# Performance work log

Measured on AMD Instinct MI355X. Metric: run time of the kernel, lower is better.

The kernel has to match this reference:

```python
import jax, jax.numpy as jnp
import numpy as np

B = 2048
F = 267          # frame_size
L = 32           # latent_size
H = 256          # hidden_size (hard-coded in module)
E = 8            # num_experts
G = 64           # gate hidden size (hard-coded)
IN0 = L + F      # decoder layer0 input (latent + frame*cond_frames)
IN1 = L + H      # decoder inter input
OUT = F          # num_future_predictions * frame_size


def _lin_init(key, out_dim, in_dim):
    # kaiming-uniform-like scale
    bound = float(np.sqrt(1.0 / in_dim))
    return jax.random.uniform(key, (out_dim, in_dim), jnp.float32, -bound, bound)


def setup_inputs() -> dict:
    key = jax.random.key(0)
    ks = jax.random.split(key, 24)
    d = {}
    d["x"] = jax.random.normal(ks[0], (B, F), jnp.float32)
    d["c"] = jax.random.normal(ks[1], (B, F), jnp.float32)
    # encoder
    d["fc1_w"] = _lin_init(ks[2], H, 2 * F); d["fc1_b"] = jnp.zeros((H,), jnp.float32)
    d["fc2_w"] = _lin_init(ks[3], H, F + H); d["fc2_b"] = jnp.zeros((H,), jnp.float32)
    d["mu_w"] = _lin_init(ks[4], L, F + H);  d["mu_b"] = jnp.zeros((L,), jnp.float32)
    d["lv_w"] = _lin_init(ks[5], L, F + H);  d["lv_b"] = jnp.zeros((L,), jnp.float32)
    # gate
    d["g0_w"] = _lin_init(ks[6], G, IN0); d["g0_b"] = jnp.zeros((G,), jnp.float32)
    d["g1_w"] = _lin_init(ks[7], G, G);   d["g1_b"] = jnp.zeros((G,), jnp.float32)
    d["g2_w"] = _lin_init(ks[8], E, G);   d["g2_b"] = jnp.zeros((E,), jnp.float32)
    # expert weights [E, in, out], biases [E, out], bias filled 0.01 as in module
    d["w0"] = jax.random.uniform(ks[9], (E, IN0, H), jnp.float32, -1, 1) * np.sqrt(1.0 / IN0)
    d["b0"] = jnp.full((E, H), 0.01, jnp.float32)
    d["w1"] = jax.random.uniform(ks[10], (E, IN1, H), jnp.float32, -1, 1) * np.sqrt(1.0 / IN1)
    d["b1"] = jnp.full((E, H), 0.01, jnp.float32)
    d["w2"] = jax.random.uniform(ks[11], (E, IN1, OUT), jnp.float32, -1, 1) * np.sqrt(1.0 / IN1)
    d["b2"] = jnp.full((E, OUT), 0.01, jnp.float32)
    return d


def reference(x, c, fc1_w, fc1_b, fc2_w, fc2_b, mu_w, mu_b, lv_w, lv_b,
              g0_w, g0_b, g1_w, g1_b, g2_w, g2_b, w0, b0, w1, b1, w2, b2):
    elu = jax.nn.elu
    # ---- encoder ----
    h1 = elu(jnp.concatenate([x, c], axis=1) @ fc1_w.T + fc1_b)
    h2 = elu(jnp.concatenate([x, h1], axis=1) @ fc2_w.T + fc2_b)
    s = jnp.concatenate([x, h2], axis=1)
    mu = s @ mu_w.T + mu_b
    logvar = s @ lv_w.T + lv_b
    eps = jax.random.normal(jax.random.key(42), mu.shape, mu.dtype)
    z = mu + eps * jnp.exp(0.5 * logvar)
    # ---- mixed decoder ----
    g = elu(jnp.concatenate([z, c], axis=1) @ g0_w.T + g0_b)
    g = elu(g @ g1_w.T + g1_b)
    coeff = jax.nn.softmax(g @ g2_w.T + g2_b, axis=1)  # [B, E]
    layer_out = c
    for (W, bvec, act) in ((w0, b0, True), (w1, b1, True), (w2, b2, False)):
        inp = jnp.concatenate([z, layer_out], axis=1)          # [B, in]
        # per-expert GEMM then coefficient mixing (same math as per-sample
        # mixed-weight bmm: coeff @ flat_weight then baddbmm)
        out = jnp.einsum('be,bi,eio->bo', coeff, inp, W, optimize=True)
        out = out + coeff @ bvec                               # mixed bias
        layer_out = elu(out) if act else out
    return (layer_out, mu, logvar)
```

## Files before the change

kernel.cpp:

```cpp
#include <hip/hip_runtime.h>
#include <math.h>
#include <stdint.h>

#define DI __device__ __forceinline__

typedef __attribute__((ext_vector_type(8))) short bf16x8;
typedef __attribute__((ext_vector_type(4))) float f32x4;
typedef __attribute__((ext_vector_type(4))) int i32x4;

DI float elu_f(float v) { return v > 0.f ? v : expm1f(v); }

DI unsigned short f2bf(float f) {
  uint32_t u = __float_as_uint(f);
  return (unsigned short)((u + 0x7FFFu + ((u >> 16) & 1u)) >> 16);
}

DI void threefry2x32(uint32_t k0, uint32_t k1, uint32_t& x0, uint32_t& x1) {
  uint32_t ks0 = k0, ks1 = k1, ks2 = k0 ^ k1 ^ 0x1BD11BDAu;
  x0 += ks0; x1 += ks1;
#define TFR(r) { x0 += x1; x1 = (x1 << r) | (x1 >> (32 - r)); x1 ^= x0; }
  TFR(13) TFR(15) TFR(26) TFR(6)   x0 += ks1; x1 += ks2 + 1u;
  TFR(17) TFR(29) TFR(16) TFR(24)  x0 += ks2; x1 += ks0 + 2u;
  TFR(13) TFR(15) TFR(26) TFR(6)   x0 += ks0; x1 += ks1 + 3u;
  TFR(17) TFR(29) TFR(16) TFR(24)  x0 += ks1; x1 += ks2 + 4u;
  TFR(13) TFR(15) TFR(26) TFR(6)   x0 += ks2; x1 += ks0 + 5u;
#undef TFR
}

DI float erfinv_f(float x) {
  float w = -logf((1.0f - x) * (1.0f + x));
  float p;
  if (w < 5.0f) {
    w -= 2.5f;
    p = 2.81022636e-08f;
    p = fmaf(p, w, 3.43273939e-07f);
    p = fmaf(p, w, -3.5233877e-06f);
    p = fmaf(p, w, -4.39150654e-06f);
    p = fmaf(p, w, 0.00021858087f);
    p = fmaf(p, w, -0.00125372503f);
    p = fmaf(p, w, -0.00417768164f);
    p = fmaf(p, w, 0.246640727f);
    p = fmaf(p, w, 1.50140941f);
  } else {
    w = sqrtf(w) - 3.0f;
    p = -0.000200214257f;
    p = fmaf(p, w, 0.000100950558f);
    p = fmaf(p, w, 0.00134934322f);
    p = fmaf(p, w, -0.00367342844f);
    p = fmaf(p, w, 0.00573950773f);
    p = fmaf(p, w, -0.0076224613f);
    p = fmaf(p, w, 0.00943887047f);
    p = fmaf(p, w, 1.00167406f);
    p = fmaf(p, w, 2.83297682f);
  }
  return p * x;
}

struct MegaArgs {
  const float *x, *c;
  const float *fc1w, *fc1b, *fc2w, *fc2b, *muw, *mub, *lvw, *lvb;
  const float *g0w, *g0b, *g1w, *g1b, *g2w, *g2b;
  const float *w0, *b0, *w1, *b1, *w2, *b2;
  unsigned short *Ax, *Axh, *Axh2, *A0, *A1, *A2;
  unsigned short *fc1t, *fc2t, *mlvt, *g0t, *g1t, *w0b, *w1b, *w2b;
  float *cf, *outY, *outMu, *outLv;
};

template <int KT, int NE, int D, bool ELU, bool OUTF32>
__global__ __launch_bounds__(128, 2)
void pipe32(const unsigned short* __restrict__ A,
            const unsigned short* __restrict__ Wt, int N,
            const float* __restrict__ bias,
            const float* __restrict__ cfp,
            unsigned short* __restrict__ Cb, int ldcb, int cb_off,
            float* __restrict__ Cf) {
  constexpr int Kp = KT * 32, TT = NE * KT;
  __shared__ float bias_s[NE * 32];
  __shared__ float cfs[(NE > 1) ? 256 : 1];
  const int tid = threadIdx.x, lane = tid & 63, wv = tid >> 6;
  const int q = lane >> 4, l16 = lane & 15;
  const int m0 = blockIdx.x * 32;
  const int n0 = blockIdx.y * 32 + wv * 16;
  const int gc = n0 + l16;
  const int wrow = (gc < N) ? gc : (N - 1);
  const unsigned short* wlane = Wt + (size_t)wrow * Kp + q * 8;

  bf16x8 ring[D];
#pragma unroll
  for (int g = 0; g < D; g++) {
    if (g < TT) {
      int e = g / KT, c = g % KT;
      ring[g] = *(const bf16x8*)(wlane + (size_t)e * N * Kp + c * 32);
    }
  }
  bf16x8 areg[2][KT];
#pragma unroll
  for (int t = 0; t < 2; t++) {
    const unsigned short* alane = A + (size_t)(m0 + t * 16 + l16) * Kp + q * 8;
#pragma unroll
    for (int c = 0; c < KT; c++) areg[t][c] = *(const bf16x8*)(alane + c * 32);
  }

  if (NE == 1) {
    if (tid < 32) {
      int col = blockIdx.y * 32 + tid;
      bias_s[tid] = (col < N) ? bias[col] : 0.f;
    }
  } else {
    for (int idx = tid; idx < NE * 32; idx += 128) {
      int e = idx >> 5, col = blockIdx.y * 32 + (idx & 31);
      bias_s[idx] = (col < N) ? bias[(size_t)e * N + col] : 0.f;
    }
    for (int idx = tid; idx < 256; idx += 128)
      cfs[idx] = cfp[(size_t)(m0 + (idx >> 3)) * 8 + (idx & 7)];
  }
  __syncthreads();

  f32x4 acc[2] = {{0.f, 0.f, 0.f, 0.f}, {0.f, 0.f, 0.f, 0.f}};
  f32x4 accF[2] = {{0.f, 0.f, 0.f, 0.f}, {0.f, 0.f, 0.f, 0.f}};
#pragma unroll
  for (int g = 0; g < TT; g++) {
    const int e = g / KT, c = g % KT;
    bf16x8 bv = ring[g % D];
    acc[0] = __builtin_amdgcn_mfma_f32_16x16x32_bf16(areg[0][c], bv, acc[0], 0, 0, 0);
    acc[1] = __builtin_amdgcn_mfma_f32_16x16x32_bf16(areg[1][c], bv, acc[1], 0, 0, 0);
    if (g + D < TT) {
      int e2 = (g + D) / KT, c2 = (g + D) % KT;
      ring[g % D] = *(const bf16x8*)(wlane + (size_t)e2 * N * Kp + c2 * 32);
    }
    if (NE > 1 && c == KT - 1) {
      float bv2 = bias_s[e * 32 + wv * 16 + l16];
#pragma unroll
      for (int t = 0; t < 2; t++)
#pragma unroll
        for (int r = 0; r < 4; r++) {
          float ce = cfs[(t * 16 + q * 4 + r) * 8 + e];
          accF[t][r] += ce * (acc[t][r] + bv2);
          acc[t][r] = 0.f;
        }
    }
  }

  if (gc < N) {
#pragma unroll
    for (int t = 0; t < 2; t++)
#pragma unroll
      for (int r = 0; r < 4; r++) {
        int row = m0 + t * 16 + q * 4 + r;
        float v = (NE > 1) ? accF[t][r] : (acc[t][r] + bias_s[wv * 16 + l16]);
        if (ELU) v = elu_f(v);
        if (OUTF32) Cf[(size_t)row * 267 + gc] = v;
        else Cb[(size_t)row * ldcb + cb_off + gc] = f2bf(v);
      }
  }
}

__global__ __launch_bounds__(256) void k_prep(MegaArgs a) {
  __shared__ __align__(16) unsigned short T[64][72];
  const int bb = blockIdx.x, tid = threadIdx.x;
  if (bb < 512) {
    for (int rr = 0; rr < 4; rr++) {
      int b = bb * 4 + rr;
      const float* xr = a.x + (size_t)b * 267;
      const float* cr = a.c + (size_t)b * 267;
      unsigned short* axr = a.Ax + (size_t)b * 544;
      for (int k = tid; k < 544; k += 256) {
        float v = (k < 267) ? xr[k] : ((k < 534) ? cr[k - 267] : 0.f);
        axr[k] = f2bf(v);
      }
      unsigned short* ahr = a.Axh + (size_t)b * 544;
      unsigned short* ah2 = a.Axh2 + (size_t)b * 544;
      for (int k = tid; k < 267; k += 256) { unsigned short v = f2bf(xr[k]); ahr[k] = v; ah2[k] = v; }
      for (int k = 523 + tid; k < 544; k += 256) { ahr[k] = 0; ah2[k] = 0; }
      unsigned short* a0r = a.A0 + (size_t)b * 320;
      for (int k = tid; k < 288; k += 256)
        a0r[32 + k] = (k < 267) ? f2bf(cr[k]) : (unsigned short)0;
    }
  } else if (bb < 1152) {
    int r = bb - 512;
    const float* src; unsigned short* dst; int Ks, Kp2;
    if (r < 256)      { src = a.fc1w + (size_t)r * 534; dst = a.fc1t + (size_t)r * 544; Ks = 534; Kp2 = 544; }
    else if (r < 512) { int n = r - 256; src = a.fc2w + (size_t)n * 523; dst = a.fc2t + (size_t)n * 544; Ks = 523; Kp2 = 544; }
    else if (r < 576) { int n = r - 512; src = (n < 32) ? (a.muw + (size_t)n * 523) : (a.lvw + (size_t)(n - 32) * 523);
                        dst = a.mlvt + (size_t)n * 544; Ks = 523; Kp2 = 544; }
    else              { int n = r - 576; src = a.g0w + (size_t)n * 299; dst = a.g0t + (size_t)n * 320; Ks = 299; Kp2 = 320; }
    for (int k = tid; k < Kp2; k += 256) dst[k] = (k < Ks) ? f2bf(src[k]) : (unsigned short)0;
  } else if (bb == 1152) {
    for (int k = tid; k < 4096; k += 256) a.g1t[k] = f2bf(a.g1w[k]);
  } else {
    int t = bb - 1153;
    const float* W; unsigned short* D; int K, N2, Kp2, ldW, e, kt, nt;
    if (t < 160)      { e = t / 20;  int lt = t % 20;  kt = lt / 4; nt = lt % 4; W = a.w0; D = a.w0b; K = 299; N2 = 256; Kp2 = 320; ldW = 256; }
    else if (t < 320) { int u = t - 160; e = u / 20; int lt = u % 20; kt = lt / 4; nt = lt % 4; W = a.w1; D = a.w1b; K = 288; N2 = 256; Kp2 = 288; ldW = 256; }
    else              { int u = t - 320; e = u / 25; int lt = u % 25; kt = lt / 5; nt = lt % 5; W = a.w2; D = a.w2b; K = 288; N2 = 267; Kp2 = 288; ldW = 267; }
    const int k0 = kt * 64, n0 = nt * 64;
    const float* We = W + (size_t)e * K * ldW;
    const int jj = tid & 63, ii0 = tid >> 6;
#pragma unroll
    for (int p = 0; p < 16; p++) {
      int i = ii0 + p * 4;
      int gk = k0 + i, gn = n0 + jj;
      float v = (gk < K && gn < N2) ? We[(size_t)gk * ldW + gn] : 0.f;
      T[jj][i] = f2bf(v);
    }
    __syncthreads();
    int j = tid >> 2, chb = tid & 3;
    int gn = n0 + j;
    if (gn < N2) {
      unsigned short* drow = D + ((size_t)e * N2 + gn) * Kp2 + k0;
#pragma unroll
      for (int s = 0; s < 2; s++) {
        int ch = chb + s * 4;
        if (k0 + ch * 8 < Kp2) {
          i32x4 v = *(i32x4*)(&T[j][ch * 8]);
          *(i32x4*)(drow + ch * 8) = v;
        }
      }
    }
  }
}

__global__ __launch_bounds__(256, 2) void k_mulv_gate(MegaArgs a) {
  __shared__ float mlvS[16 * 65];
  __shared__ __align__(16) unsigned short A0p[16 * 328];
  __shared__ __align__(16) unsigned short gaB[16 * 72];
  __shared__ __align__(16) unsigned short g1B[64 * 72];
  __shared__ float g2wT[64 * 8];
  __shared__ float gB[16 * 65];
  __shared__ float lg[16 * 8];
  const int tid = threadIdx.x, lane = tid & 63, wid = tid >> 6;
  const int q = lane >> 4, l16 = lane & 15;
  const int m0 = blockIdx.x * 16;
  const int cl = wid * 16 + l16;

  const unsigned short* alane = a.Axh2 + (size_t)(m0 + l16) * 544 + q * 8;
  const unsigned short* wlA = a.mlvt + (size_t)cl * 544 + q * 8;
  bf16x8 ring[8];
#pragma unroll
  for (int g = 0; g < 8; g++) ring[g] = *(const bf16x8*)(wlA + g * 32);
  bf16x8 areg[17];
#pragma unroll
  for (int c = 0; c < 17; c++) areg[c] = *(const bf16x8*)(alane + c * 32);
  f32x4 acc = {0.f, 0.f, 0.f, 0.f};
#pragma unroll
  for (int g = 0; g < 17; g++) {
    acc = __builtin_amdgcn_mfma_f32_16x16x32_bf16(areg[g], ring[g % 8], acc, 0, 0, 0);
    if (g + 8 < 17) ring[g % 8] = *(const bf16x8*)(wlA + (g + 8) * 32);
  }
#pragma unroll
  for (int r = 0; r < 4; r++) mlvS[(q * 4 + r) * 65 + cl] = acc[r];
  for (int idx = tid; idx < 576; idx += 256) {
    int row = idx / 36, ch = 4 + idx % 36;
    *(i32x4*)(A0p + row * 328 + ch * 8) =
        *(const i32x4*)(a.A0 + (size_t)(m0 + row) * 320 + ch * 8);
  }
  if (tid < 16) { i32x4 z4 = {0, 0, 0, 0}; *(i32x4*)(A0p + tid * 328 + 320) = z4; }
  for (int idx = tid; idx < 512; idx += 256) {
    int row = idx >> 3, ch = idx & 7;
    *(i32x4*)(g1B + row * 72 + ch * 8) = *(const i32x4*)(a.g1t + (size_t)row * 64 + ch * 8);
  }
  for (int idx = tid; idx < 512; idx += 256)
    g2wT[(idx & 63) * 8 + (idx >> 6)] = a.g2w[idx];
  __syncthreads();

  {
    const int m = tid >> 4, j0 = (tid & 15) * 2, R = m0 + m;
#pragma unroll
    for (int jj = 0; jj < 2; jj++) {
      int j = j0 + jj;
      float mu = mlvS[m * 65 + j] + a.mub[j];
      float lvv = mlvS[m * 65 + j + 32] + a.lvb[j];
      uint32_t x0 = 0u, x1 = (uint32_t)(R * 32 + j);
      threefry2x32(0u, 42u, x0, x1);
      uint32_t bits = x0 ^ x1;
      float f = __uint_as_float((bits >> 9) | 0x3F800000u) - 1.0f;
      const float lo = -0.99999994039535522461f;
      float u = fmaf(f, 2.0f, lo);
      u = fmaxf(u, lo);
      float eps = 1.41421356237f * erfinv_f(u);
      float z = fmaf(eps, expf(0.5f * lvv), mu);
      a.outMu[(size_t)R * 32 + j] = mu;
      a.outLv[(size_t)R * 32 + j] = lvv;
      unsigned short zb = f2bf(z);
      A0p[m * 328 + j] = zb;
      a.A0[(size_t)R * 320 + j] = zb;
      a.A1[(size_t)R * 288 + j] = zb;
      a.A2[(size_t)R * 288 + j] = zb;
    }
  }
  __syncthreads();

  const unsigned short* wlC = a.g0t + (size_t)cl * 320 + q * 8;
  bf16x8 ring2[8];
#pragma unroll
  for (int g = 0; g < 8; g++) ring2[g] = *(const bf16x8*)(wlC + g * 32);
  f32x4 accC = {0.f, 0.f, 0.f, 0.f};
#pragma unroll
  for (int g = 0; g < 10; g++) {
    bf16x8 av = *(const bf16x8*)(A0p + l16 * 328 + g * 32 + q * 8);
    accC = __builtin_amdgcn_mfma_f32_16x16x32_bf16(av, ring2[g % 8], accC, 0, 0, 0);
    if (g + 8 < 10) ring2[g % 8] = *(const bf16x8*)(wlC + (g + 8) * 32);
  }
  {
    float bc = a.g0b[cl];
#pragma unroll
    for (int r = 0; r < 4; r++)
      gaB[(q * 4 + r) * 72 + cl] = f2bf(elu_f(accC[r] + bc));
  }
  __syncthreads();

  f32x4 accD = {0.f, 0.f, 0.f, 0.f};
#pragma unroll
  for (int tau = 0; tau < 2; tau++) {
    bf16x8 av = *(const bf16x8*)(gaB + l16 * 72 + tau * 32 + q * 8);
    bf16x8 bv = *(const bf16x8*)(g1B + cl * 72 + tau * 32 + q * 8);
    accD = __builtin_amdgcn_mfma_f32_16x16x32_bf16(av, bv, accD, 0, 0, 0);
  }
  {
    float bc = a.g1b[cl];
#pragma unroll
    for (int r = 0; r < 4; r++)
      gB[(q * 4 + r) * 65 + cl] = elu_f(accD[r] + bc);
  }
  __syncthreads();

  if (tid < 128) {
    int r = tid >> 3, e = tid & 7;
    float d = a.g2b[e];
#pragma unroll 8
    for (int k = 0; k < 64; k++) d = fmaf(gB[r * 65 + k], g2wT[k * 8 + e], d);
    lg[r * 8 + e] = d;
  }
  __syncthreads();
  if (tid < 16) {
    float mx = lg[tid * 8];
#pragma unroll
    for (int e2 = 1; e2 < 8; e2++) mx = fmaxf(mx, lg[tid * 8 + e2]);
    float s = 0.f, ex[8];
#pragma unroll
    for (int e2 = 0; e2 < 8; e2++) { ex[e2] = expf(lg[tid * 8 + e2] - mx); s += ex[e2]; }
    float inv = 1.f / s;
#pragma unroll
    for (int e2 = 0; e2 < 8; e2++) a.cf[(size_t)(m0 + tid) * 8 + e2] = ex[e2] * inv;
  }
}

extern "C" void kernel_launch(void* const* d_in, const int* in_sizes, int n_in,
                              void* d_out, int out_size, void* d_ws, size_t ws_size,
                              hipStream_t stream) {
  (void)in_sizes; (void)n_in; (void)out_size; (void)ws_size;
  float* out = (float*)d_out;
  float* ws = (float*)d_ws;

  MegaArgs a;
  a.x    = (const float*)d_in[0];
  a.c    = (const float*)d_in[1];
  a.fc1w = (const float*)d_in[2];  a.fc1b = (const float*)d_in[3];
  a.fc2w = (const float*)d_in[4];  a.fc2b = (const float*)d_in[5];
  a.muw  = (const float*)d_in[6];  a.mub  = (const float*)d_in[7];
  a.lvw  = (const float*)d_in[8];  a.lvb  = (const float*)d_in[9];
  a.g0w  = (const float*)d_in[10]; a.g0b  = (const float*)d_in[11];
  a.g1w  = (const float*)d_in[12]; a.g1b  = (const float*)d_in[13];
  a.g2w  = (const float*)d_in[14]; a.g2b  = (const float*)d_in[15];
  a.w0   = (const float*)d_in[16]; a.b0   = (const float*)d_in[17];
  a.w1   = (const float*)d_in[18]; a.b1   = (const float*)d_in[19];
  a.w2   = (const float*)d_in[20]; a.b2   = (const float*)d_in[21];

  a.outY  = out;
  a.outMu = out + 2048 * 267;
  a.outLv = a.outMu + 2048 * 32;

  a.Ax   = (unsigned short*)(ws);
  a.Axh  = (unsigned short*)(ws + 557056);
  a.Axh2 = (unsigned short*)(ws + 1114112);
  a.A0   = (unsigned short*)(ws + 1671168);
  a.A1   = (unsigned short*)(ws + 1998848);
  a.A2   = (unsigned short*)(ws + 2293760);
  a.fc1t = (unsigned short*)(ws + 2588672);
  a.fc2t = (unsigned short*)(ws + 2658304);
  a.mlvt = (unsigned short*)(ws + 2727936);
  a.g0t  = (unsigned short*)(ws + 2745344);
  a.g1t  = (unsigned short*)(ws + 2755584);
  a.w0b  = (unsigned short*)(ws + 2757632);
  a.w1b  = (unsigned short*)(ws + 3085312);
  a.w2b  = (unsigned short*)(ws + 3380224);
  a.cf   = ws + 3687808;

  dim3 blkP(256), blkG(128);
  k_prep<<<1673, blkP, 0, stream>>>(a);
  pipe32<17, 1, 12, true, false><<<dim3(64, 8), blkG, 0, stream>>>(
      a.Ax, a.fc1t, 256, a.fc1b, nullptr, a.Axh, 544, 267, nullptr);
  pipe32<17, 1, 12, true, false><<<dim3(64, 8), blkG, 0, stream>>>(
      a.Axh, a.fc2t, 256, a.fc2b, nullptr, a.Axh2, 544, 267, nullptr);
  k_mulv_gate<<<128, blkP, 0, stream>>>(a);
  pipe32<10, 8, 12, true, false><<<dim3(64, 8), blkG, 0, stream>>>(
      a.A0, a.w0b, 256, a.b0, a.cf, a.A1, 288, 32, nullptr);
  pipe32<9, 8, 12, true, false><<<dim3(64, 8), blkG, 0, stream>>>(
      a.A1, a.w1b, 256, a.b1, a.cf, a.A2, 288, 32, nullptr);
  pipe32<9, 8, 12, false, true><<<dim3(64, 9), blkG, 0, stream>>>(
      a.A2, a.w2b, 267, a.b2, a.cf, nullptr, 0, 0, a.outY);
}
```

Before: 175.8 us.

## Fuse encoder, gate, and expert decoder layers into one per-row-block kernel

Replaces the separate encoder GEMMs, mu/logvar+gate kernel, and three expert-mix GEMM launches with a single kernel that keeps each 16-row block's activations in shared memory across all layers. This removes intermediate global round-trips, launch gaps, and the redundant activation staging in the prep kernel. In exchange the grid shrinks to 128 blocks, reducing parallelism, and every block rereads all expert weights from cache.

```diff
diff --git a/kernel.cpp b/kernel.cpp
--- a/kernel.cpp
+++ b/kernel.cpp
@@ -7,6 +7,8 @@
 typedef __attribute__((ext_vector_type(8))) short bf16x8;
 typedef __attribute__((ext_vector_type(4))) float f32x4;
 typedef __attribute__((ext_vector_type(4))) int i32x4;
+
+#define MFMA16(av, bv, acc) __builtin_amdgcn_mfma_f32_16x16x32_bf16(av, bv, acc, 0, 0, 0)
 
 DI float elu_f(float v) { return v > 0.f ? v : expm1f(v); }
 
@@ -66,95 +68,6 @@
   float *cf, *outY, *outMu, *outLv;
 };
 
-template <int KT, int NE, int D, bool ELU, bool OUTF32>
-__global__ __launch_bounds__(128, 2)
-void pipe32(const unsigned short* __restrict__ A,
-            const unsigned short* __restrict__ Wt, int N,
-            const float* __restrict__ bias,
-            const float* __restrict__ cfp,
-            unsigned short* __restrict__ Cb, int ldcb, int cb_off,
-            float* __restrict__ Cf) {
-  constexpr int Kp = KT * 32, TT = NE * KT;
-  __shared__ float bias_s[NE * 32];
-  __shared__ float cfs[(NE > 1) ? 256 : 1];
-  const int tid = threadIdx.x, lane = tid & 63, wv = tid >> 6;
-  const int q = lane >> 4, l16 = lane & 15;
-  const int m0 = blockIdx.x * 32;
-  const int n0 = blockIdx.y * 32 + wv * 16;
-  const int gc = n0 + l16;
-  const int wrow = (gc < N) ? gc : (N - 1);
-  const unsigned short* wlane = Wt + (size_t)wrow * Kp + q * 8;
-
-  bf16x8 ring[D];
-#pragma unroll
-  for (int g = 0; g < D; g++) {
-    if (g < TT) {
-      int e = g / KT, c = g % KT;
-      ring[g] = *(const bf16x8*)(wlane + (size_t)e * N * Kp + c * 32);
-    }
-  }
-  bf16x8 areg[2][KT];
-#pragma unroll
-  for (int t = 0; t < 2; t++) {
-    const unsigned short* alane = A + (size_t)(m0 + t * 16 + l16) * Kp + q * 8;
-#pragma unroll
-    for (int c = 0; c < KT; c++) areg[t][c] = *(const bf16x8*)(alane + c * 32);
-  }
-
-  if (NE == 1) {
-    if (tid < 32) {
-      int col = blockIdx.y * 32 + tid;
-      bias_s[tid] = (col < N) ? bias[col] : 0.f;
-    }
-  } else {
-    for (int idx = tid; idx < NE * 32; idx += 128) {
-      int e = idx >> 5, col = blockIdx.y * 32 + (idx & 31);
-      bias_s[idx] = (col < N) ? bias[(size_t)e * N + col] : 0.f;
-    }
-    for (int idx = tid; idx < 256; idx += 128)
-      cfs[idx] = cfp[(size_t)(m0 + (idx >> 3)) * 8 + (idx & 7)];
-  }
-  __syncthreads();
-
-  f32x4 acc[2] = {{0.f, 0.f, 0.f, 0.f}, {0.f, 0.f, 0.f, 0.f}};
-  f32x4 accF[2] = {{0.f, 0.f, 0.f, 0.f}, {0.f, 0.f, 0.f, 0.f}};
-#pragma unroll
-  for (int g = 0; g < TT; g++) {
-    const int e = g / KT, c = g % KT;
-    bf16x8 bv = ring[g % D];
-    acc[0] = __builtin_amdgcn_mfma_f32_16x16x32_bf16(areg[0][c], bv, acc[0], 0, 0, 0);
-    acc[1] = __builtin_amdgcn_mfma_f32_16x16x32_bf16(areg[1][c], bv, acc[1], 0, 0, 0);
-    if (g + D < TT) {
-      int e2 = (g + D) / KT, c2 = (g + D) % KT;
-      ring[g % D] = *(const bf16x8*)(wlane + (size_t)e2 * N * Kp + c2 * 32);
-    }
-    if (NE > 1 && c == KT - 1) {
-      float bv2 = bias_s[e * 32 + wv * 16 + l16];
-#pragma unroll
-      for (int t = 0; t < 2; t++)
-#pragma unroll
-        for (int r = 0; r < 4; r++) {
-          float ce = cfs[(t * 16 + q * 4 + r) * 8 + e];
-          accF[t][r] += ce * (acc[t][r] + bv2);
-          acc[t][r] = 0.f;
-        }
-    }
-  }
-
-  if (gc < N) {
-#pragma unroll
-    for (int t = 0; t < 2; t++)
-#pragma unroll
-      for (int r = 0; r < 4; r++) {
-        int row = m0 + t * 16 + q * 4 + r;
-        float v = (NE > 1) ? accF[t][r] : (acc[t][r] + bias_s[wv * 16 + l16]);
-        if (ELU) v = elu_f(v);
-        if (OUTF32) Cf[(size_t)row * 267 + gc] = v;
-        else Cb[(size_t)row * ldcb + cb_off + gc] = f2bf(v);
-      }
-  }
-}
-
 __global__ __launch_bounds__(256) void k_prep(MegaArgs a) {
   __shared__ __align__(16) unsigned short T[64][72];
   const int bb = blockIdx.x, tid = threadIdx.x;
@@ -168,10 +81,6 @@
         float v = (k < 267) ? xr[k] : ((k < 534) ? cr[k - 267] : 0.f);
         axr[k] = f2bf(v);
       }
-      unsigned short* ahr = a.Axh + (size_t)b * 544;
-      unsigned short* ah2 = a.Axh2 + (size_t)b * 544;
-      for (int k = tid; k < 267; k += 256) { unsigned short v = f2bf(xr[k]); ahr[k] = v; ah2[k] = v; }
-      for (int k = 523 + tid; k < 544; k += 256) { ahr[k] = 0; ah2[k] = 0; }
       unsigned short* a0r = a.A0 + (size_t)b * 320;
       for (int k = tid; k < 288; k += 256)
         a0r[32 + k] = (k < 267) ? f2bf(cr[k]) : (unsigned short)0;
@@ -220,56 +129,117 @@
   }
 }
 
-__global__ __launch_bounds__(256, 2) void k_mulv_gate(MegaArgs a) {
-  __shared__ float mlvS[16 * 65];
-  __shared__ __align__(16) unsigned short A0p[16 * 328];
-  __shared__ __align__(16) unsigned short gaB[16 * 72];
-  __shared__ __align__(16) unsigned short g1B[64 * 72];
-  __shared__ float g2wT[64 * 8];
-  __shared__ float gB[16 * 65];
-  __shared__ float lg[16 * 8];
-  const int tid = threadIdx.x, lane = tid & 63, wid = tid >> 6;
+__global__ __launch_bounds__(512, 2) void k_chain(MegaArgs a) {
+  __shared__ __align__(16) unsigned short sAxh[16][552];
+  __shared__ __align__(16) unsigned short sA0[16][328];
+  __shared__ __align__(16) unsigned short sA1[16][296];
+  __shared__ float sMlv[16][65];
+  __shared__ __align__(16) unsigned short sGa[16][72];
+  __shared__ float sGb[16][65];
+  __shared__ float sG2[512];
+  __shared__ float sLg[128];
+  __shared__ float sCf[16][8];
+
+  const int tid = threadIdx.x, lane = tid & 63, w = tid >> 6;
   const int q = lane >> 4, l16 = lane & 15;
   const int m0 = blockIdx.x * 16;
-  const int cl = wid * 16 + l16;
-
-  const unsigned short* alane = a.Axh2 + (size_t)(m0 + l16) * 544 + q * 8;
-  const unsigned short* wlA = a.mlvt + (size_t)cl * 544 + q * 8;
-  bf16x8 ring[8];
-#pragma unroll
-  for (int g = 0; g < 8; g++) ring[g] = *(const bf16x8*)(wlA + g * 32);
-  bf16x8 areg[17];
-#pragma unroll
-  for (int c = 0; c < 17; c++) areg[c] = *(const bf16x8*)(alane + c * 32);
-  f32x4 acc = {0.f, 0.f, 0.f, 0.f};
-#pragma unroll
-  for (int g = 0; g < 17; g++) {
-    acc = __builtin_amdgcn_mfma_f32_16x16x32_bf16(areg[g], ring[g % 8], acc, 0, 0, 0);
-    if (g + 8 < 17) ring[g % 8] = *(const bf16x8*)(wlA + (g + 8) * 32);
-  }
-#pragma unroll
-  for (int r = 0; r < 4; r++) mlvS[(q * 4 + r) * 65 + cl] = acc[r];
-  for (int idx = tid; idx < 576; idx += 256) {
-    int row = idx / 36, ch = 4 + idx % 36;
-    *(i32x4*)(A0p + row * 328 + ch * 8) =
-        *(const i32x4*)(a.A0 + (size_t)(m0 + row) * 320 + ch * 8);
-  }
-  if (tid < 16) { i32x4 z4 = {0, 0, 0, 0}; *(i32x4*)(A0p + tid * 328 + 320) = z4; }
-  for (int idx = tid; idx < 512; idx += 256) {
-    int row = idx >> 3, ch = idx & 7;
-    *(i32x4*)(g1B + row * 72 + ch * 8) = *(const i32x4*)(a.g1t + (size_t)row * 64 + ch * 8);
-  }
-  for (int idx = tid; idx < 512; idx += 256)
-    g2wT[(idx & 63) * 8 + (idx >> 6)] = a.g2w[idx];
+
+  for (int idx = tid; idx < 16 * 34; idx += 512) {
+    int row = idx / 34, ch = idx % 34;
+    *(i32x4*)(&sAxh[row][ch * 8]) =
+        *(const i32x4*)(a.Ax + (size_t)(m0 + row) * 544 + ch * 8);
+  }
+  for (int idx = tid; idx < 16 * 29; idx += 512) sAxh[idx / 29][523 + idx % 29] = 0;
+  for (int idx = tid; idx < 16 * 36; idx += 512) {
+    int row = idx / 36, ch = idx % 36;
+    *(i32x4*)(&sA0[row][32 + ch * 8]) =
+        *(const i32x4*)(a.A0 + (size_t)(m0 + row) * 320 + 32 + ch * 8);
+  }
+  sG2[(tid & 63) * 8 + (tid >> 6)] = a.g2w[tid];
   __syncthreads();
 
   {
-    const int m = tid >> 4, j0 = (tid & 15) * 2, R = m0 + m;
-#pragma unroll
-    for (int jj = 0; jj < 2; jj++) {
+    const int n0 = w * 32, c0 = n0 + l16, c1 = n0 + 16 + l16;
+    const unsigned short* ap  = a.Ax   + (size_t)(m0 + l16) * 544 + q * 8;
+    const unsigned short* wp0 = a.fc1t + (size_t)c0 * 544 + q * 8;
+    const unsigned short* wp1 = a.fc1t + (size_t)c1 * 544 + q * 8;
+    bf16x8 r0[8], r1[8], ra[4];
+#pragma unroll
+    for (int i = 0; i < 8; i++) { r0[i] = *(const bf16x8*)(wp0 + i * 32); r1[i] = *(const bf16x8*)(wp1 + i * 32); }
+#pragma unroll
+    for (int i = 0; i < 4; i++) ra[i] = *(const bf16x8*)(ap + i * 32);
+    f32x4 acc0 = {0.f, 0.f, 0.f, 0.f}, acc1 = {0.f, 0.f, 0.f, 0.f};
+#pragma unroll
+    for (int c = 0; c < 17; c++) {
+      bf16x8 av = ra[c & 3];
+      acc0 = MFMA16(av, r0[c & 7], acc0);
+      acc1 = MFMA16(av, r1[c & 7], acc1);
+      if (c + 4 < 17) ra[c & 3] = *(const bf16x8*)(ap + (c + 4) * 32);
+      if (c + 8 < 17) { r0[c & 7] = *(const bf16x8*)(wp0 + (c + 8) * 32);
+                        r1[c & 7] = *(const bf16x8*)(wp1 + (c + 8) * 32); }
+    }
+    float b0v = a.fc1b[c0], b1v = a.fc1b[c1];
+#pragma unroll
+    for (int r = 0; r < 4; r++) {
+      int row = q * 4 + r;
+      sAxh[row][267 + c0] = f2bf(elu_f(acc0[r] + b0v));
+      sAxh[row][267 + c1] = f2bf(elu_f(acc1[r] + b1v));
+    }
+  }
+  __syncthreads();
+
+  {
+    const int n0 = w * 32, c0 = n0 + l16, c1 = n0 + 16 + l16;
+    const unsigned short* wp0 = a.fc2t + (size_t)c0 * 544 + q * 8;
+    const unsigned short* wp1 = a.fc2t + (size_t)c1 * 544 + q * 8;
+    bf16x8 r0[8], r1[8];
+#pragma unroll
+    for (int i = 0; i < 8; i++) { r0[i] = *(const bf16x8*)(wp0 + i * 32); r1[i] = *(const bf16x8*)(wp1 + i * 32); }
+    f32x4 acc0 = {0.f, 0.f, 0.f, 0.f}, acc1 = {0.f, 0.f, 0.f, 0.f};
+#pragma unroll
+    for (int c = 0; c < 17; c++) {
+      bf16x8 av = *(const bf16x8*)(&sAxh[l16][c * 32 + q * 8]);
+      acc0 = MFMA16(av, r0[c & 7], acc0);
+      acc1 = MFMA16(av, r1[c & 7], acc1);
+      if (c + 8 < 17) { r0[c & 7] = *(const bf16x8*)(wp0 + (c + 8) * 32);
+                        r1[c & 7] = *(const bf16x8*)(wp1 + (c + 8) * 32); }
+    }
+    __syncthreads();
+    float b0v = a.fc2b[c0], b1v = a.fc2b[c1];
+#pragma unroll
+    for (int r = 0; r < 4; r++) {
+      int row = q * 4 + r;
+      sAxh[row][267 + c0] = f2bf(elu_f(acc0[r] + b0v));
+      sAxh[row][267 + c1] = f2bf(elu_f(acc1[r] + b1v));
+    }
+  }
+  __syncthreads();
+
+  if (w < 4) {
+    const int cl = w * 16 + l16;
+    const unsigned short* wp = a.mlvt + (size_t)cl * 544 + q * 8;
+    bf16x8 rw[8];
+#pragma unroll
+    for (int i = 0; i < 8; i++) rw[i] = *(const bf16x8*)(wp + i * 32);
+    f32x4 acc = {0.f, 0.f, 0.f, 0.f};
+#pragma unroll
+    for (int c = 0; c < 17; c++) {
+      bf16x8 av = *(const bf16x8*)(&sAxh[l16][c * 32 + q * 8]);
+      acc = MFMA16(av, rw[c & 7], acc);
+      if (c + 8 < 17) rw[c & 7] = *(const bf16x8*)(wp + (c + 8) * 32);
+    }
+#pragma unroll
+    for (int r = 0; r < 4; r++) sMlv[q * 4 + r][cl] = acc[r];
+  }
+  __syncthreads();
+
+  if (tid < 128) {
+    const int m = tid >> 3, j0 = (tid & 7) * 4, R = m0 + m;
+#pragma unroll
+    for (int jj = 0; jj < 4; jj++) {
       int j = j0 + jj;
-      float mu = mlvS[m * 65 + j] + a.mub[j];
-      float lvv = mlvS[m * 65 + j + 32] + a.lvb[j];
+      float mu = sMlv[m][j] + a.mub[j];
+      float lvv = sMlv[m][j + 32] + a.lvb[j];
       uint32_t x0 = 0u, x1 = (uint32_t)(R * 32 + j);
       threefry2x32(0u, 42u, x0, x1);
       uint32_t bits = x0 ^ x1;
@@ -282,66 +252,169 @@
       a.outMu[(size_t)R * 32 + j] = mu;
       a.outLv[(size_t)R * 32 + j] = lvv;
       unsigned short zb = f2bf(z);
-      A0p[m * 328 + j] = zb;
-      a.A0[(size_t)R * 320 + j] = zb;
-      a.A1[(size_t)R * 288 + j] = zb;
-      a.A2[(size_t)R * 288 + j] = zb;
-    }
-  }
-  __syncthreads();
-
-  const unsigned short* wlC = a.g0t + (size_t)cl * 320 + q * 8;
-  bf16x8 ring2[8];
-#pragma unroll
-  for (int g = 0; g < 8; g++) ring2[g] = *(const bf16x8*)(wlC + g * 32);
-  f32x4 accC = {0.f, 0.f, 0.f, 0.f};
-#pragma unroll
-  for (int g = 0; g < 10; g++) {
-    bf16x8 av = *(const bf16x8*)(A0p + l16 * 328 + g * 32 + q * 8);
-    accC = __builtin_amdgcn_mfma_f32_16x16x32_bf16(av, ring2[g % 8], accC, 0, 0, 0);
-    if (g + 8 < 10) ring2[g % 8] = *(const bf16x8*)(wlC + (g + 8) * 32);
-  }
-  {
+      sA0[m][j] = zb;
+      sA1[m][j] = zb;
+    }
+  }
+  __syncthreads();
+
+  if (w < 4) {
+    const int cl = w * 16 + l16;
+    const unsigned short* wp = a.g0t + (size_t)cl * 320 + q * 8;
+    bf16x8 rw[8];
+#pragma unroll
+    for (int i = 0; i < 8; i++) rw[i] = *(const bf16x8*)(wp + i * 32);
+    f32x4 acc = {0.f, 0.f, 0.f, 0.f};
+#pragma unroll
+    for (int c = 0; c < 10; c++) {
+      bf16x8 av = *(const bf16x8*)(&sA0[l16][c * 32 + q * 8]);
+      acc = MFMA16(av, rw[c & 7], acc);
+      if (c + 8 < 10) rw[c & 7] = *(const bf16x8*)(wp + (c + 8) * 32);
+    }
     float bc = a.g0b[cl];
 #pragma unroll
-    for (int r = 0; r < 4; r++)
-      gaB[(q * 4 + r) * 72 + cl] = f2bf(elu_f(accC[r] + bc));
-  }
-  __syncthreads();
-
-  f32x4 accD = {0.f, 0.f, 0.f, 0.f};
-#pragma unroll
-  for (int tau = 0; tau < 2; tau++) {
-    bf16x8 av = *(const bf16x8*)(gaB + l16 * 72 + tau * 32 + q * 8);
-    bf16x8 bv = *(const bf16x8*)(g1B + cl * 72 + tau * 32 + q * 8);
-    accD = __builtin_amdgcn_mfma_f32_16x16x32_bf16(av, bv, accD, 0, 0, 0);
-  }
-  {
+    for (int r = 0; r < 4; r++) sGa[q * 4 + r][cl] = f2bf(elu_f(acc[r] + bc));
+  }
+  __syncthreads();
+
+  if (w < 4) {
+    const int cl = w * 16 + l16;
+    bf16x8 bv0 = *(const bf16x8*)(a.g1t + (size_t)cl * 64 + q * 8);
+    bf16x8 bv1 = *(const bf16x8*)(a.g1t + (size_t)cl * 64 + 32 + q * 8);
+    bf16x8 av0 = *(const bf16x8*)(&sGa[l16][q * 8]);
+    bf16x8 av1 = *(const bf16x8*)(&sGa[l16][32 + q * 8]);
+    f32x4 acc = {0.f, 0.f, 0.f, 0.f};
+    acc = MFMA16(av0, bv0, acc);
+    acc = MFMA16(av1, bv1, acc);
     float bc = a.g1b[cl];
 #pragma unroll
-    for (int r = 0; r < 4; r++)
-      gB[(q * 4 + r) * 65 + cl] = elu_f(accD[r] + bc);
-  }
-  __syncthreads();
-
+    for (int r = 0; r < 4; r++) sGb[q * 4 + r][cl] = elu_f(acc[r] + bc);
+  }
+  __syncthreads();
   if (tid < 128) {
     int r = tid >> 3, e = tid & 7;
     float d = a.g2b[e];
 #pragma unroll 8
-    for (int k = 0; k < 64; k++) d = fmaf(gB[r * 65 + k], g2wT[k * 8 + e], d);
-    lg[r * 8 + e] = d;
+    for (int k = 0; k < 64; k++) d = fmaf(sGb[r][k], sG2[k * 8 + e], d);
+    sLg[r * 8 + e] = d;
   }
   __syncthreads();
   if (tid < 16) {
-    float mx = lg[tid * 8];
-#pragma unroll
-    for (int e2 = 1; e2 < 8; e2++) mx = fmaxf(mx, lg[tid * 8 + e2]);
+    float mx = sLg[tid * 8];
+#pragma unroll
+    for (int e2 = 1; e2 < 8; e2++) mx = fmaxf(mx, sLg[tid * 8 + e2]);
     float s = 0.f, ex[8];
 #pragma unroll
-    for (int e2 = 0; e2 < 8; e2++) { ex[e2] = expf(lg[tid * 8 + e2] - mx); s += ex[e2]; }
+    for (int e2 = 0; e2 < 8; e2++) { ex[e2] = expf(sLg[tid * 8 + e2] - mx); s += ex[e2]; }
     float inv = 1.f / s;
 #pragma unroll
-    for (int e2 = 0; e2 < 8; e2++) a.cf[(size_t)(m0 + tid) * 8 + e2] = ex[e2] * inv;
+    for (int e2 = 0; e2 < 8; e2++) sCf[tid][e2] = ex[e2] * inv;
+  }
+  __syncthreads();
+
+  {
+    const int n0 = w * 32, c0 = n0 + l16, c1 = n0 + 16 + l16;
+    const unsigned short* wp0 = a.w0b + (size_t)c0 * 320 + q * 8;
+    const unsigned short* wp1 = a.w0b + (size_t)c1 * 320 + q * 8;
+    bf16x8 r0[10], r1[10];
+#pragma unroll
+    for (int c = 0; c < 10; c++) { r0[c] = *(const bf16x8*)(wp0 + c * 32); r1[c] = *(const bf16x8*)(wp1 + c * 32); }
+    f32x4 accF0 = {0.f, 0.f, 0.f, 0.f}, accF1 = {0.f, 0.f, 0.f, 0.f};
+    for (int e = 0; e < 8; e++) {
+      const unsigned short* nx0 = wp0 + (size_t)(e + 1) * 81920;
+      const unsigned short* nx1 = wp1 + (size_t)(e + 1) * 81920;
+      f32x4 acc0 = {0.f, 0.f, 0.f, 0.f}, acc1 = {0.f, 0.f, 0.f, 0.f};
+#pragma unroll
+      for (int c = 0; c < 10; c++) {
+        bf16x8 av = *(const bf16x8*)(&sA0[l16][c * 32 + q * 8]);
+        acc0 = MFMA16(av, r0[c], acc0);
+        acc1 = MFMA16(av, r1[c], acc1);
+        if (e < 7) { r0[c] = *(const bf16x8*)(nx0 + c * 32); r1[c] = *(const bf16x8*)(nx1 + c * 32); }
+      }
+      float bv0 = a.b0[e * 256 + c0], bv1 = a.b0[e * 256 + c1];
+#pragma unroll
+      for (int r = 0; r < 4; r++) {
+        float ce = sCf[q * 4 + r][e];
+        accF0[r] += ce * (acc0[r] + bv0);
+        accF1[r] += ce * (acc1[r] + bv1);
+      }
+    }
+    __syncthreads();
+#pragma unroll
+    for (int r = 0; r < 4; r++) {
+      int row = q * 4 + r;
+      sA1[row][32 + c0] = f2bf(elu_f(accF0[r]));
+      sA1[row][32 + c1] = f2bf(elu_f(accF1[r]));
+    }
+  }
+  __syncthreads();
+
+  {
+    const int n0 = w * 32, c0 = n0 + l16, c1 = n0 + 16 + l16;
+    const unsigned short* wp0 = a.w1b + (size_t)c0 * 288 + q * 8;
+    const unsigned short* wp1 = a.w1b + (size_t)c1 * 288 + q * 8;
+    bf16x8 r0[9], r1[9];
+#pragma unroll
+    for (int c = 0; c < 9; c++) { r0[c] = *(const bf16x8*)(wp0 + c * 32); r1[c] = *(const bf16x8*)(wp1 + c * 32); }
+    f32x4 accF0 = {0.f, 0.f, 0.f, 0.f}, accF1 = {0.f, 0.f, 0.f, 0.f};
+    for (int e = 0; e < 8; e++) {
+      const unsigned short* nx0 = wp0 + (size_t)(e + 1) * 73728;
+      const unsigned short* nx1 = wp1 + (size_t)(e + 1) * 73728;
+      f32x4 acc0 = {0.f, 0.f, 0.f, 0.f}, acc1 = {0.f, 0.f, 0.f, 0.f};
+#pragma unroll
+      for (int c = 0; c < 9; c++) {
+        bf16x8 av = *(const bf16x8*)(&sA1[l16][c * 32 + q * 8]);
+        acc0 = MFMA16(av, r0[c], acc0);
+        acc1 = MFMA16(av, r1[c], acc1);
+        if (e < 7) { r0[c] = *(const bf16x8*)(nx0 + c * 32); r1[c] = *(const bf16x8*)(nx1 + c * 32); }
+      }
+      float bv0 = a.b1[e * 256 + c0], bv1 = a.b1[e * 256 + c1];
+#pragma unroll
+      for (int r = 0; r < 4; r++) {
+        float ce = sCf[q * 4 + r][e];
+        accF0[r] += ce * (acc0[r] + bv0);
+        accF1[r] += ce * (acc1[r] + bv1);
+      }
+    }
+    __syncthreads();
+#pragma unroll
+    for (int r = 0; r < 4; r++) {
+      int row = q * 4 + r;
+      sA1[row][32 + c0] = f2bf(elu_f(accF0[r]));
+      sA1[row][32 + c1] = f2bf(elu_f(accF1[r]));
+    }
+  }
+  __syncthreads();
+
+  for (int j = w; j < 17; j += 8) {
+    const int col = j * 16 + l16;
+    const int vcol = (col < 267) ? col : 266;
+    const unsigned short* wp = a.w2b + (size_t)vcol * 288 + q * 8;
+    bf16x8 rw[9];
+#pragma unroll
+    for (int c = 0; c < 9; c++) rw[c] = *(const bf16x8*)(wp + c * 32);
+    f32x4 accF = {0.f, 0.f, 0.f, 0.f};
+    for (int e = 0; e < 8; e++) {
+      const unsigned short* nx = wp + (size_t)(e + 1) * 76896;
+      f32x4 acc = {0.f, 0.f, 0.f, 0.f};
+#pragma unroll
+      for (int c = 0; c < 9; c++) {
+        bf16x8 av = *(const bf16x8*)(&sA1[l16][c * 32 + q * 8]);
+        acc = MFMA16(av, rw[c], acc);
+        if (e < 7) rw[c] = *(const bf16x8*)(nx + c * 32);
+      }
+      float bv = a.b2[e * 267 + vcol];
+#pragma unroll
+      for (int r = 0; r < 4; r++) {
+        float ce = sCf[q * 4 + r][e];
+        accF[r] += ce * (acc[r] + bv);
+      }
+    }
+    if (col < 267) {
+#pragma unroll
+      for (int r = 0; r < 4; r++)
+        a.outY[(size_t)(m0 + q * 4 + r) * 267 + col] = accF[r];
+    }
   }
 }
 
@@ -386,17 +459,6 @@
   a.w2b  = (unsigned short*)(ws + 3380224);
   a.cf   = ws + 3687808;
 
-  dim3 blkP(256), blkG(128);
-  k_prep<<<1673, blkP, 0, stream>>>(a);
-  pipe32<17, 1, 12, true, false><<<dim3(64, 8), blkG, 0, stream>>>(
-      a.Ax, a.fc1t, 256, a.fc1b, nullptr, a.Axh, 544, 267, nullptr);
-  pipe32<17, 1, 12, true, false><<<dim3(64, 8), blkG, 0, stream>>>(
-      a.Axh, a.fc2t, 256, a.fc2b, nullptr, a.Axh2, 544, 267, nullptr);
-  k_mulv_gate<<<128, blkP, 0, stream>>>(a);
-  pipe32<10, 8, 12, true, false><<<dim3(64, 8), blkG, 0, stream>>>(
-      a.A0, a.w0b, 256, a.b0, a.cf, a.A1, 288, 32, nullptr);
-  pipe32<9, 8, 12, true, false><<<dim3(64, 8), blkG, 0, stream>>>(
-      a.A1, a.w1b, 256, a.b1, a.cf, a.A2, 288, 32, nullptr);
-  pipe32<9, 8, 12, false, true><<<dim3(64, 9), blkG, 0, stream>>>(
-      a.A2, a.w2b, 267, a.b2, a.cf, nullptr, 0, 0, a.outY);
-}
+  k_prep<<<1673, 256, 0, stream>>>(a);
+  k_chain<<<128, 512, 0, stream>>>(a);
+}
```

Result: slower. 213.9 us (+21.7%).
